# Kernel optimization log

Measured on AMD Instinct MI355X. Metric: run time of the kernel, lower is better.

Reference implementation:

```python
import jax, jax.numpy as jnp
import numpy as np

UNITS = 1024
INPUT_DIM = 512
BATCH = 2048

def setup_inputs() -> dict:
    key = jax.random.key(0)
    k1, k2, k3, k4 = jax.random.split(key, 4)
    return {
        "inputs": jax.random.normal(k1, (BATCH, INPUT_DIM), dtype=jnp.float32),
        "h_tm1": jax.random.normal(k2, (BATCH, UNITS), dtype=jnp.float32),
        "c_tm1": jax.random.normal(k3, (BATCH, UNITS), dtype=jnp.float32),
        # keras 'random_normal' initializer: stddev 0.05
        "kernel": jax.random.normal(k4, (UNITS + INPUT_DIM, 4 * UNITS), dtype=jnp.float32) * 0.05,
    }

def reference(inputs, h_tm1, c_tm1, kernel):
    # z = concat([h, x]) @ kernel ; kernel rows: [units (h-block); input_dim (x-block)]
    z = jnp.concatenate([h_tm1, inputs], axis=-1) @ kernel  # [B, 4*units]
    z0, z1, z2, z3 = jnp.split(z, 4, axis=-1)
    i = jax.nn.sigmoid(z0)
    f = jax.nn.sigmoid(z1)
    c_tilde = jnp.tanh(z2)
    o = jax.nn.sigmoid(z3)
    c = f * c_tm1 + i * c_tilde
    h = o * jnp.tanh(c)
    return (h, c)
```

## Files before the change

kernel.cpp:

```cpp
#include <hip/hip_runtime.h>
#include <hip/hip_bf16.h>
#include <stdint.h>

#define UNITS 1024
#define IDIM  512
#define BATCH 2048
#define KTOT  1536
#define NGATE 4096
#define NKK   48
#define NITER 24

typedef short bf16x8 __attribute__((ext_vector_type(8)));
typedef float f32x4  __attribute__((ext_vector_type(4)));

union P8 { bf16x8 v; __hip_bfloat16 e[8]; };


#define NBLK_A 1536
#define NBLK_T 3072

__global__ __launch_bounds__(256) void prep(
    const float* __restrict__ x, const float* __restrict__ h,
    const float* __restrict__ W,
    bf16x8* __restrict__ A2, bf16x8* __restrict__ Wt2) {
  __shared__ float tile[32][65];
  const int tid = threadIdx.x;
  if (blockIdx.x < NBLK_A) {
    const int gid = blockIdx.x * 256 + tid;
    const int f  = gid >> 6;
    const int L  = gid & 63;
    const int ii = f / NKK;
    const int kk = f - ii * NKK;
    const int r  = ii * 16 + (L & 15);
    const int k  = kk * 32 + (L >> 4) * 8;
    const float* src = (k < UNITS) ? h + (size_t)r * UNITS + k
                                   : x + (size_t)r * IDIM + (k - UNITS);
    const float4 v0 = ((const float4*)src)[0];
    const float4 v1 = ((const float4*)src)[1];
    P8 o;
    o.e[0] = __float2bfloat16(v0.x); o.e[1] = __float2bfloat16(v0.y);
    o.e[2] = __float2bfloat16(v0.z); o.e[3] = __float2bfloat16(v0.w);
    o.e[4] = __float2bfloat16(v1.x); o.e[5] = __float2bfloat16(v1.y);
    o.e[6] = __float2bfloat16(v1.z); o.e[7] = __float2bfloat16(v1.w);
    A2[gid] = o.v;
  } else {
    const int b  = blockIdx.x - NBLK_A;
    const int kb = b >> 7;
    const int nb = b & 127;
    const int k0 = kb * 64, n0 = nb * 32;
    const int n4 = (tid & 7) * 4;
    const int kk = tid >> 3;
#pragma unroll
    for (int rr = 0; rr < 64; rr += 32) {
      const float4 v = *(const float4*)(W + (size_t)(k0 + kk + rr) * NGATE + n0 + n4);
      tile[n4 + 0][kk + rr] = v.x; tile[n4 + 1][kk + rr] = v.y;
      tile[n4 + 2][kk + rr] = v.z; tile[n4 + 3][kk + rr] = v.w;
    }
    __syncthreads();
    const int L    = tid & 63;
    const int half = tid >> 6;
    const int jl   = half >> 1;
    const int kl   = half & 1;
    const int nloc = (L & 15) + jl * 16;
    const int kloc = kl * 32 + (L >> 4) * 8;
    P8 o;
#pragma unroll
    for (int j = 0; j < 8; ++j) o.e[j] = __float2bfloat16(tile[nloc][kloc + j]);
    const int jj = (n0 >> 4) + jl;
    const int kc = (k0 >> 5) + kl;
    Wt2[(size_t)(jj * NKK + kc) * 64 + L] = o.v;
  }
}

__global__ __launch_bounds__(256, 2) void lstm_gemm(
    const bf16x8* __restrict__ A2,
    const bf16x8* __restrict__ Wt2,
    const float* __restrict__ c_tm1,
    float* __restrict__ out) {
  const int tid  = threadIdx.x;
  const int w    = tid >> 6;
  const int lane = tid & 63;
  const int quad = lane >> 4;
  const int m16  = lane & 15;
  const int wr   = w >> 1;
  const int wu   = w & 1;

  const int mb = blockIdx.x >> 5;
  const int ub = blockIdx.x & 31;
  const int m0 = mb * 128;
  const int u0 = ub * 32;

  size_t aoff[4], boff[4];
  const int ii0 = mb * 8 + wr * 4;
#pragma unroll
  for (int i = 0; i < 4; ++i)
    aoff[i] = (size_t)((ii0 + i) * NKK) * 64 + lane;
#pragma unroll
  for (int g = 0; g < 4; ++g) {
    const int jj = g * 64 + ub * 2 + wu;
    boff[g] = (size_t)(jj * NKK) * 64 + lane;
  }

  f32x4 acc[4][4];
#pragma unroll
  for (int i = 0; i < 4; ++i)
#pragma unroll
    for (int g = 0; g < 4; ++g) {
      f32x4 z = {0.f, 0.f, 0.f, 0.f};
      acc[i][g] = z;
    }

  bf16x8 a[2][4][2], b[2][4][2];

#pragma unroll
  for (int t = 0; t < 2; ++t) {
#pragma unroll
    for (int i = 0; i < 4; ++i) a[0][i][t] = A2[aoff[i] + t * 64];
#pragma unroll
    for (int g = 0; g < 4; ++g) b[0][g][t] = Wt2[boff[g] + t * 64];
  }

#pragma unroll 2
  for (int it = 0; it < NITER; ++it) {
    const int cur = it & 1;
    const int nxt = cur ^ 1;
    if (it < NITER - 1) {
      const int kk = (it + 1) * 2;
#pragma unroll
      for (int t = 0; t < 2; ++t) {
#pragma unroll
        for (int i = 0; i < 4; ++i) a[nxt][i][t] = A2[aoff[i] + (kk + t) * 64];
#pragma unroll
        for (int g = 0; g < 4; ++g) b[nxt][g][t] = Wt2[boff[g] + (kk + t) * 64];
      }
    }
#pragma unroll
    for (int t = 0; t < 2; ++t)
#pragma unroll
      for (int g = 0; g < 4; ++g)
#pragma unroll
        for (int i = 0; i < 4; ++i)
          acc[i][g] = __builtin_amdgcn_mfma_f32_16x16x32_bf16(a[cur][i][t],
                                                              b[cur][g][t],
                                                              acc[i][g], 0, 0, 0);
  }

  const int u = u0 + wu * 16 + m16;
#pragma unroll
  for (int i = 0; i < 4; ++i)
#pragma unroll
    for (int reg = 0; reg < 4; ++reg) {
      const int r = m0 + wr * 64 + i * 16 + quad * 4 + reg;
      const float z0 = acc[i][0][reg];
      const float z1 = acc[i][1][reg];
      const float z2 = acc[i][2][reg];
      const float z3 = acc[i][3][reg];
      const float ig = 1.f / (1.f + __expf(-z0));
      const float fg = 1.f / (1.f + __expf(-z1));
      const float ct = 1.f - 2.f / (__expf(2.f * z2) + 1.f);
      const float og = 1.f / (1.f + __expf(-z3));
      const float cc = fg * c_tm1[(size_t)r * UNITS + u] + ig * ct;
      const float hh = og * (1.f - 2.f / (__expf(2.f * cc) + 1.f));
      out[(size_t)r * UNITS + u] = hh;
      out[(size_t)BATCH * UNITS + (size_t)r * UNITS + u] = cc;
    }
}

__global__ __launch_bounds__(256) void lstm_naive(
    const float* __restrict__ x, const float* __restrict__ h,
    const float* __restrict__ c_tm1, const float* __restrict__ W,
    float* __restrict__ out) {
  int idx = blockIdx.x * 256 + threadIdx.x;
  int r = idx / UNITS;
  int u = idx % UNITS;
  float z[4] = {0.f, 0.f, 0.f, 0.f};
  for (int k = 0; k < KTOT; ++k) {
    float a = (k < UNITS) ? h[(size_t)r * UNITS + k] : x[(size_t)r * IDIM + k - UNITS];
#pragma unroll
    for (int g = 0; g < 4; ++g)
      z[g] += a * W[(size_t)k * NGATE + g * UNITS + u];
  }
  float ig = 1.f / (1.f + __expf(-z[0]));
  float fg = 1.f / (1.f + __expf(-z[1]));
  float ct = 1.f - 2.f / (__expf(2.f * z[2]) + 1.f);
  float og = 1.f / (1.f + __expf(-z[3]));
  float cc = fg * c_tm1[(size_t)r * UNITS + u] + ig * ct;
  float hh = og * (1.f - 2.f / (__expf(2.f * cc) + 1.f));
  out[(size_t)r * UNITS + u] = hh;
  out[(size_t)BATCH * UNITS + (size_t)r * UNITS + u] = cc;
}

extern "C" void kernel_launch(void* const* d_in, const int* in_sizes, int n_in,
                              void* d_out, int out_size, void* d_ws, size_t ws_size,
                              hipStream_t stream) {
  const float* x = (const float*)d_in[0];
  const float* h = (const float*)d_in[1];
  const float* c = (const float*)d_in[2];
  const float* W = (const float*)d_in[3];
  float* out = (float*)d_out;

  const size_t needA  = (size_t)BATCH * KTOT * sizeof(__hip_bfloat16);
  const size_t needWt = (size_t)NGATE * KTOT * sizeof(__hip_bfloat16);
  if (ws_size < needA + needWt) {
    hipLaunchKernelGGL(lstm_naive, dim3((BATCH * UNITS) / 256), dim3(256), 0, stream,
                       x, h, c, W, out);
    return;
  }

  bf16x8* A2  = (bf16x8*)d_ws;
  bf16x8* Wt2 = (bf16x8*)((char*)d_ws + needA);

  hipLaunchKernelGGL(prep, dim3(NBLK_A + NBLK_T), dim3(256), 0, stream, x, h, W, A2, Wt2);
  hipLaunchKernelGGL(lstm_gemm, dim3(512), dim3(256), 0, stream, A2, Wt2, c, out);
}
```

Baseline: 124.7 us.

## Stage shared B operand tiles in LDS via asynchronous global-to-LDS loads

The weight operand is now copied into a double-buffered LDS tile with global_load_lds, so the two wave rows that use the same B fragments read it once per block instead of each wave fetching it from global memory. Each wave then reads B from LDS before its MFMAs, and A keeps its register double-buffering. The aim is to halve global and L2 traffic for the weight operand. In exchange it adds a block-wide barrier every K iteration, extra LDS reads, and drops the unroll-2 pragma on the main loop.

```diff
diff --git a/kernel.cpp b/kernel.cpp
--- a/kernel.cpp
+++ b/kernel.cpp
@@ -12,6 +12,9 @@
 
 typedef short bf16x8 __attribute__((ext_vector_type(8)));
 typedef float f32x4  __attribute__((ext_vector_type(4)));
+
+#define AS3(p) ((__attribute__((address_space(3))) void*)(p))
+#define AS1(p) ((const __attribute__((address_space(1))) void*)(p))
 
 union P8 { bf16x8 v; __hip_bfloat16 e[8]; };
 
@@ -77,6 +80,8 @@
     const bf16x8* __restrict__ Wt2,
     const float* __restrict__ c_tm1,
     float* __restrict__ out) {
+  __shared__ __attribute__((aligned(128))) char lds[2 * 16384];
+
   const int tid  = threadIdx.x;
   const int w    = tid >> 6;
   const int lane = tid & 63;
@@ -90,16 +95,23 @@
   const int m0 = mb * 128;
   const int u0 = ub * 32;
 
-  size_t aoff[4], boff[4];
+  const bf16x8* bsrc[4];
+  int bdst[4];
+#pragma unroll
+  for (int s = 0; s < 4; ++s) {
+    const int idx = s * 4 + w;
+    const int f   = idx >> 1;
+    const int t   = idx & 1;
+    const int jj  = (f >> 1) * 64 + ub * 2 + (f & 1);
+    bsrc[s] = Wt2 + (size_t)(jj * NKK + t) * 64 + lane;
+    bdst[s] = idx * 1024;
+  }
+
+  size_t aoff[4];
   const int ii0 = mb * 8 + wr * 4;
 #pragma unroll
   for (int i = 0; i < 4; ++i)
     aoff[i] = (size_t)((ii0 + i) * NKK) * 64 + lane;
-#pragma unroll
-  for (int g = 0; g < 4; ++g) {
-    const int jj = g * 64 + ub * 2 + wu;
-    boff[g] = (size_t)(jj * NKK) * 64 + lane;
-  }
 
   f32x4 acc[4][4];
 #pragma unroll
@@ -110,39 +122,46 @@
       acc[i][g] = z;
     }
 
-  bf16x8 a[2][4][2], b[2][4][2];
-
-#pragma unroll
-  for (int t = 0; t < 2; ++t) {
+  bf16x8 a[2][4][2];
+
+#pragma unroll
+  for (int s = 0; s < 4; ++s)
+    __builtin_amdgcn_global_load_lds(AS1(bsrc[s]), AS3(lds + bdst[s]), 16, 0, 0);
+#pragma unroll
+  for (int t = 0; t < 2; ++t)
 #pragma unroll
     for (int i = 0; i < 4; ++i) a[0][i][t] = A2[aoff[i] + t * 64];
-#pragma unroll
-    for (int g = 0; g < 4; ++g) b[0][g][t] = Wt2[boff[g] + t * 64];
-  }
-
-#pragma unroll 2
+  __syncthreads();
+
   for (int it = 0; it < NITER; ++it) {
     const int cur = it & 1;
     const int nxt = cur ^ 1;
     if (it < NITER - 1) {
       const int kk = (it + 1) * 2;
 #pragma unroll
-      for (int t = 0; t < 2; ++t) {
-#pragma unroll
-        for (int i = 0; i < 4; ++i) a[nxt][i][t] = A2[aoff[i] + (kk + t) * 64];
-#pragma unroll
-        for (int g = 0; g < 4; ++g) b[nxt][g][t] = Wt2[boff[g] + (kk + t) * 64];
-      }
-    }
-#pragma unroll
-    for (int t = 0; t < 2; ++t)
+      for (int s = 0; s < 4; ++s)
+        __builtin_amdgcn_global_load_lds(AS1(bsrc[s] + (size_t)kk * 64),
+                                         AS3(lds + nxt * 16384 + bdst[s]), 16, 0, 0);
+#pragma unroll
+      for (int t = 0; t < 2; ++t)
+#pragma unroll
+        for (int i = 0; i < 4; ++i) a[nxt][i][t] = A2[aoff[i] + (size_t)(kk + t) * 64];
+    }
+    const char* bbuf = lds + cur * 16384;
+#pragma unroll
+    for (int t = 0; t < 2; ++t) {
+      bf16x8 b[4];
 #pragma unroll
       for (int g = 0; g < 4; ++g)
+        b[g] = *(const bf16x8*)(bbuf + ((g * 2 + wu) * 2 + t) * 1024 + lane * 16);
+#pragma unroll
+      for (int g = 0; g < 4; ++g)
 #pragma unroll
         for (int i = 0; i < 4; ++i)
-          acc[i][g] = __builtin_amdgcn_mfma_f32_16x16x32_bf16(a[cur][i][t],
-                                                              b[cur][g][t],
+          acc[i][g] = __builtin_amdgcn_mfma_f32_16x16x32_bf16(a[cur][i][t], b[g],
                                                               acc[i][g], 0, 0, 0);
+    }
+    __syncthreads();
   }
 
   const int u = u0 + wu * 16 + m16;
```

Result: no change. 127.2 us (+2.0%).
